# Performance work log

Hardware: AMD Instinct MI355X
Metric: run time of the kernel (lower is better)

The kernel has to match this reference:

```python
import jax, jax.numpy as jnp
import numpy as np

N, E, G = 40000, 400000, 64
IN, ED, HID, HEADS, OUT = 2, 18, 64, 4, 3

def _glorot(key, shape):
    fan_in = shape[0]
    return jax.random.normal(key, shape, dtype=jnp.float32) / np.float32(np.sqrt(fan_in))

def setup_inputs():
    key = jax.random.key(0)
    ks = jax.random.split(key, 32)
    d1 = HEADS * HID  # 256
    return {
        "x": jax.random.normal(ks[0], (N, IN), jnp.float32),
        "edge_index": jax.random.randint(ks[1], (2, E), 0, N),
        "edge_attr": jax.random.normal(ks[2], (E, ED), jnp.float32),
        "batch": jnp.sort(jax.random.randint(ks[3], (N,), 0, G)),
        # conv1: TransformerConv(2 -> 64, heads=4, concat=True, beta=True, edge_dim=18)
        "Wq1": _glorot(ks[4], (IN, d1)), "bq1": jnp.zeros((d1,), jnp.float32),
        "Wk1": _glorot(ks[5], (IN, d1)), "bk1": jnp.zeros((d1,), jnp.float32),
        "Wv1": _glorot(ks[6], (IN, d1)), "bv1": jnp.zeros((d1,), jnp.float32),
        "We1": _glorot(ks[7], (ED, d1)),
        "Wskip1": _glorot(ks[8], (IN, d1)), "bskip1": jnp.zeros((d1,), jnp.float32),
        "Wbeta1": _glorot(ks[9], (3 * d1, 1)),
        # conv2: TransformerConv(256 -> 64, heads=1, concat=False, beta=True, edge_dim=18)
        "Wq2": _glorot(ks[10], (d1, HID)), "bq2": jnp.zeros((HID,), jnp.float32),
        "Wk2": _glorot(ks[11], (d1, HID)), "bk2": jnp.zeros((HID,), jnp.float32),
        "Wv2": _glorot(ks[12], (d1, HID)), "bv2": jnp.zeros((HID,), jnp.float32),
        "We2": _glorot(ks[13], (ED, HID)),
        "Wskip2": _glorot(ks[14], (d1, HID)), "bskip2": jnp.zeros((HID,), jnp.float32),
        "Wbeta2": _glorot(ks[15], (3 * HID, 1)),
        "Wlin": _glorot(ks[16], (HID, OUT)), "blin": jnp.zeros((OUT,), jnp.float32),
    }

def _tconv(x, src, dst, edge_attr, Wq, bq, Wk, bk, Wv, bv, We, Wskip, bskip, Wbeta, H, C, concat):
    # PyG TransformerConv with edge_dim, beta=True, root_weight=True (eval: dropout off)
    n = x.shape[0]
    q = (x @ Wq + bq).reshape(n, H, C)
    k = (x @ Wk + bk).reshape(n, H, C)
    v = (x @ Wv + bv).reshape(n, H, C)
    e = (edge_attr @ We).reshape(-1, H, C)              # [E,H,C]
    kj = k[src] + e                                      # key_j + edge
    alpha = jnp.einsum('ehc,ehc->eh', q[dst], kj) * (1.0 / (C ** 0.5))  # [E,H]
    # segment softmax over destination nodes
    amax = jax.ops.segment_max(alpha, dst, num_segments=n)
    ex = jnp.exp(alpha - amax[dst])
    den = jax.ops.segment_sum(ex, dst, num_segments=n)
    w = ex / (den[dst] + 1e-16)
    msg = (v[src] + e) * w[:, :, None]                   # [E,H,C]
    out = jax.ops.segment_sum(msg, dst, num_segments=n)  # [N,H,C]
    out = out.reshape(n, H * C) if concat else out.mean(axis=1)
    # beta-gated skip connection
    xr = x @ Wskip + bskip
    beta = jax.nn.sigmoid(jnp.concatenate([out, xr, out - xr], axis=-1) @ Wbeta)
    return beta * xr + (1.0 - beta) * out

def reference(x, edge_index, edge_attr, batch, Wq1, bq1, Wk1, bk1, Wv1, bv1, We1, Wskip1, bskip1, Wbeta1, Wq2, bq2, Wk2, bk2, Wv2, bv2, We2, Wskip2, bskip2, Wbeta2, Wlin, blin):
    src, dst = edge_index[0], edge_index[1]
    h = jax.nn.relu(_tconv(x, src, dst, edge_attr, Wq1, bq1, Wk1, bk1, Wv1, bv1, We1, Wskip1, bskip1, Wbeta1, HEADS, HID, True))
    h = jax.nn.relu(_tconv(h, src, dst, edge_attr, Wq2, bq2, Wk2, bk2, Wv2, bv2, We2, Wskip2, bskip2, Wbeta2, 1, HID, False))
    # global mean pool per graph
    s = jax.ops.segment_sum(h, batch, num_segments=G)
    cnt = jax.ops.segment_sum(jnp.ones((h.shape[0], 1), h.dtype), batch, num_segments=G)
    pooled = s / jnp.maximum(cnt, 1.0)
    return pooled @ Wlin + blin
```

## Files before the change

### kernel.cpp

```cpp
#include <hip/hip_runtime.h>
#include <hip/hip_fp16.h>

#define N_NODES 40000
#define N_EDGES 400000
#define N_GRAPHS 64
#define D1 256
#define HIDC 64
#define NHEADS 4
#define EDIM 18
#define EPAD 20
#define OUTF 3
#define APAD 264

typedef _Float16 f16x8 __attribute__((ext_vector_type(8)));
typedef float f32x4 __attribute__((ext_vector_type(4)));

__global__ void prep_w(const float* __restrict__ Wq, const float* __restrict__ bq,
                       const float* __restrict__ Wk, const float* __restrict__ bk,
                       const float* __restrict__ Wv, const float* __restrict__ bv,
                       const float* __restrict__ Ws, const float* __restrict__ bs,
                       const float* __restrict__ We2,
                       const float* __restrict__ Wq1, const float* __restrict__ bq1,
                       const float* __restrict__ Wk1, const float* __restrict__ bk1,
                       const float* __restrict__ We1,
                       __half* __restrict__ Bt, float* __restrict__ bias,
                       float* __restrict__ cbuf) {
    int c = blockIdx.x, k = threadIdx.x;
    if (c < 256) {
        int m = c >> 6, d = c & 63;
        const float* W = (m == 0) ? Wq : (m == 1) ? Wk : (m == 2) ? Wv : Ws;
        Bt[c * 256 + k] = __float2half(W[k * 64 + d]);
        if (k == 0) {
            const float* b = (m == 0) ? bq : (m == 1) ? bk : (m == 2) ? bv : bs;
            bias[c] = b[d];
        }
    } else if (c < 288) {
        int j = c - 256;
        float s = 0.f;
        if (j < EDIM)
            for (int cc = 0; cc < 64; ++cc) s += Wq[k * 64 + cc] * We2[j * 64 + cc];
        Bt[c * 256 + k] = __float2half(s);
        if (k == 0) {
            float b = 0.f;
            if (j < EDIM)
                for (int cc = 0; cc < 64; ++cc) b += bq[cc] * We2[j * 64 + cc];
            bias[c] = b;
        }
    } else {
        int t = k;
        if (t < 36) {
            int h = t / 9, r = t % 9, a = r / 3, b = r % 3;
            const float* A = (a == 0) ? Wq1 : (a == 1) ? Wq1 + D1 : bq1;
            const float* B = (b == 0) ? Wk1 : (b == 1) ? Wk1 + D1 : bk1;
            float s = 0.f;
            for (int cc = 0; cc < 64; ++cc) s += A[h * 64 + cc] * B[h * 64 + cc];
            cbuf[h * 63 + a * 3 + b] = s;
        } else if (t < 252) {
            int i = t - 36;
            int h = i / 54, rr = (i % 54) / 18, j = i % 18;
            const float* A = (rr == 0) ? Wq1 : (rr == 1) ? Wq1 + D1 : bq1;
            float s = 0.f;
            for (int cc = 0; cc < 64; ++cc) s += A[h * 64 + cc] * We1[j * D1 + h * 64 + cc];
            cbuf[h * 63 + 9 + rr * 18 + j] = s;
        }
    }
}

__global__ void initA(const float* __restrict__ x, const float* __restrict__ cbuf,
                      float* __restrict__ coef, float* __restrict__ acc1,
                      float* __restrict__ acc2, float* __restrict__ out2,
                      int* __restrict__ deg, float* __restrict__ pooled,
                      int* __restrict__ gs, int* __restrict__ ge) {
    int t = blockIdx.x * 256 + threadIdx.x;
    acc1[t] = 0.f;
    {
        int n = t / 84, r = t % 84, h = r / 21, c = r % 21;
        const float* cb = cbuf + h * 63;
        float x0 = x[2 * n], x1 = x[2 * n + 1], o;
        if (c < 3) o = x0 * cb[c] + x1 * cb[3 + c] + cb[6 + c];
        else { int j = c - 3; o = x0 * cb[9 + j] + x1 * cb[27 + j] + cb[45 + j]; }
        coef[t] = o;
    }
    if (t < N_NODES * 64) out2[t] = 0.f;
    if (t < N_NODES * 20) acc2[t] = 0.f;
    if (t < N_NODES) deg[t] = 0;
    if (t < N_GRAPHS * HIDC) pooled[t] = 0.f;
    if (t < N_GRAPHS) { gs[t] = 0; ge[t] = 0; }
}

__global__ void hist_kernel(const int* __restrict__ ei, int* __restrict__ deg,
                            const int* __restrict__ batch, int* __restrict__ gs,
                            int* __restrict__ ge) {
    int e = blockIdx.x * 256 + threadIdx.x;
    if (e < N_EDGES) atomicAdd(&deg[ei[N_EDGES + e]], 1);
    int n = e;
    if (n < N_NODES) {
        int b = batch[n];
        if (n == 0) gs[b] = 0;
        else { int pb = batch[n - 1]; if (pb != b) { ge[pb] = n; gs[b] = n; } }
        if (n == N_NODES - 1) ge[b] = N_NODES;
    }
}

__global__ void scanA(const int* __restrict__ deg, int* __restrict__ bsum) {
    __shared__ int s[256];
    int b = blockIdx.x, t = threadIdx.x;
    s[t] = (t < 160) ? deg[b * 160 + t] : 0;
    __syncthreads();
    for (int off = 128; off; off >>= 1) {
        if (t < off) s[t] += s[t + off];
        __syncthreads();
    }
    if (t == 0) bsum[b] = s[0];
}

__global__ void scanB(const int* __restrict__ bsum, int* __restrict__ boff) {
    __shared__ int s[256];
    int t = threadIdx.x;
    int v = (t < 250) ? bsum[t] : 0;
    s[t] = v;
    __syncthreads();
    for (int off = 1; off < 256; off <<= 1) {
        int add = (t >= off) ? s[t - off] : 0;
        __syncthreads();
        s[t] += add;
        __syncthreads();
    }
    if (t < 250) boff[t] = s[t] - v;
}

__global__ void scanC(const int* __restrict__ deg, const int* __restrict__ boff,
                      int* __restrict__ cursor) {
    __shared__ int s[256];
    int b = blockIdx.x, t = threadIdx.x;
    int v = (t < 160) ? deg[b * 160 + t] : 0;
    s[t] = v;
    __syncthreads();
    for (int off = 1; off < 256; off <<= 1) {
        int add = (t >= off) ? s[t - off] : 0;
        __syncthreads();
        s[t] += add;
        __syncthreads();
    }
    if (t < 160) cursor[b * 160 + t] = boff[b] + s[t] - v;
}

__global__ void scatterE(const int* __restrict__ ei, const float* __restrict__ ea,
                         const float* __restrict__ x, int* __restrict__ cursor,
                         int* __restrict__ src_s, int* __restrict__ dst_s,
                         float* __restrict__ ea_s) {
    int e = blockIdx.x * 256 + threadIdx.x;
    if (e >= N_EDGES) return;
    int src = ei[e], dst = ei[N_EDGES + e];
    const float2* sr = (const float2*)(ea + (size_t)e * EDIM);
    float2 s0 = sr[0], s1 = sr[1], s2 = sr[2], s3 = sr[3], s4 = sr[4],
           s5 = sr[5], s6 = sr[6], s7 = sr[7], s8 = sr[8];
    float2 xv = *(const float2*)(x + (size_t)src * 2);
    int p = atomicAdd(&cursor[dst], 1);
    src_s[p] = src;
    dst_s[p] = dst;
    float4* drow = (float4*)(ea_s + (size_t)p * EPAD);
    drow[0] = make_float4(s0.x, s0.y, s1.x, s1.y);
    drow[1] = make_float4(s2.x, s2.y, s3.x, s3.y);
    drow[2] = make_float4(s4.x, s4.y, s5.x, s5.y);
    drow[3] = make_float4(s6.x, s6.y, s7.x, s7.y);
    drow[4] = make_float4(s8.x, s8.y, xv.x, xv.y);
}

__global__ void strip1f(const int* __restrict__ dst_s, const float* __restrict__ ea_s,
                        const float* __restrict__ coef, float* __restrict__ acc1) {
    int t = threadIdx.x;
    int strip = blockIdx.x * 2 + (t >> 7);
    int l = t & 127;
    int h = l >> 5, comp = l & 31;
    bool active = comp < 21;
    int voff = (comp == 0) ? 18 : (comp == 1) ? 19 : (comp >= 3 ? comp - 3 : 0);
    bool isone = (comp == 2);
    int cidx = h * 21 + comp;
    int p0 = strip * 16;
    int dsts[16]; float v[16];
    #pragma unroll
    for (int j = 0; j < 16; ++j) dsts[j] = dst_s[p0 + j];
    #pragma unroll
    for (int j = 0; j < 16; ++j)
        v[j] = active ? (isone ? 1.f : ea_s[(size_t)(p0 + j) * EPAD + voff]) : 0.f;
    int prev = dsts[0];
    float c = active ? coef[(size_t)prev * 84 + cidx] : 0.f;
    float acc = 0.f;
    #pragma unroll
    for (int j = 0; j < 16; ++j) {
        if (dsts[j] != prev) {
            if (active) atomicAdd(&acc1[(size_t)prev * 84 + cidx], acc);
            acc = 0.f; prev = dsts[j];
            c = active ? coef[(size_t)prev * 84 + cidx] : 0.f;
        }
        float prod = c * v[j];
        #pragma unroll
        for (int off = 16; off; off >>= 1) prod += __shfl_xor(prod, off);
        float w = __expf(prod * 0.125f);
        acc += w * v[j];
    }
    if (active) atomicAdd(&acc1[(size_t)prev * 84 + cidx], acc);
}

__global__ void finalize1x(const float* __restrict__ x, const float* __restrict__ acc1,
                           const float* __restrict__ Wv, const float* __restrict__ bv,
                           const float* __restrict__ We, const float* __restrict__ Wskip,
                           const float* __restrict__ bskip, const float* __restrict__ Wbeta,
                           __half* __restrict__ h1f) {
    __shared__ float red[4][4];
    int nb = blockIdx.x * 4;
    int t = threadIdx.x;
    int h = t >> 6;
    float wv0 = Wv[t], wv1 = Wv[D1 + t], bvv = bv[t];
    float we[EDIM];
    #pragma unroll
    for (int j = 0; j < EDIM; ++j) we[j] = We[j * D1 + t];
    float ws0 = Wskip[t], ws1 = Wskip[D1 + t], bsv = bskip[t];
    float wb0 = Wbeta[t], wb1 = Wbeta[D1 + t], wb2 = Wbeta[2 * D1 + t];
    float o[4], xr[4], part[4];
    #pragma unroll
    for (int i = 0; i < 4; ++i) {
        int node = nb + i;
        const float* a = acc1 + (size_t)node * 84 + h * 21;
        float l = a[2];
        float oo = a[0] * wv0 + a[1] * wv1 + l * bvv;
        #pragma unroll
        for (int j = 0; j < EDIM; ++j) oo += a[3 + j] * we[j];
        oo /= (l + 1e-16f);
        float x0 = x[node * 2], x1 = x[node * 2 + 1];
        xr[i] = x0 * ws0 + x1 * ws1 + bsv;
        o[i] = oo;
        part[i] = oo * wb0 + xr[i] * wb1 + (oo - xr[i]) * wb2;
    }
    #pragma unroll
    for (int off = 32; off; off >>= 1) {
        #pragma unroll
        for (int i = 0; i < 4; ++i) part[i] += __shfl_xor(part[i], off);
    }
    if ((t & 63) == 0) {
        #pragma unroll
        for (int i = 0; i < 4; ++i) red[h][i] = part[i];
    }
    __syncthreads();
    #pragma unroll
    for (int i = 0; i < 4; ++i) {
        float tot = red[0][i] + red[1][i] + red[2][i] + red[3][i];
        float beta = 1.f / (1.f + __expf(-tot));
        h1f[(size_t)(nb + i) * D1 + t] =
            __float2half(fmaxf(beta * xr[i] + (1.f - beta) * o[i], 0.f));
    }
}

__device__ __forceinline__ void nl2_store(int c, int gr, float v,
        float* __restrict__ q2, float* __restrict__ k2, __half* __restrict__ v2h,
        float* __restrict__ xr2, float* __restrict__ qe) {
    if (c < 256) {
        int m = c >> 6, d = c & 63;
        if (m == 0)      q2[(size_t)gr * 64 + d] = v;
        else if (m == 1) k2[(size_t)gr * 64 + d] = v;
        else if (m == 2) v2h[(size_t)gr * 64 + d] = __float2half(v);
        else             xr2[(size_t)gr * 64 + d] = v;
    } else {
        qe[(size_t)gr * 32 + (c - 256)] = v;
    }
}

__global__ __launch_bounds__(256) void nl2_mfma(
        const __half* __restrict__ h1f, const __half* __restrict__ Bt,
        const float* __restrict__ bias,
        float* __restrict__ q2, float* __restrict__ k2,
        __half* __restrict__ v2h, float* __restrict__ xr2,
        float* __restrict__ qe) {
    __shared__ _Float16 As[64 * APAD];
    int t = threadIdx.x;
    int row0 = blockIdx.x * 64;
    const float4* gsrc = (const float4*)(h1f + (size_t)row0 * 256);
    #pragma unroll
    for (int i = 0; i < 8; ++i) {
        int li = i * 256 + t;
        int r = li >> 5, c8 = li & 31;
        *(float4*)(As + r * APAD + c8 * 8) = gsrc[li];
    }
    __syncthreads();
    int wave = t >> 6, lane = t & 63, quad = lane >> 4, mm = lane & 15;
    const _Float16* Bp = (const _Float16*)Bt;
    for (int ct = wave; ct < 18; ct += 4) {
        int c0 = ct * 16 + mm;
        const _Float16* b0 = Bp + (size_t)c0 * 256 + quad * 8;
        f16x8 b[8];
        #pragma unroll
        for (int s = 0; s < 8; ++s) b[s] = *(const f16x8*)(b0 + s * 32);
        float bz = bias[c0];
        #pragma unroll
        for (int rt = 0; rt < 4; ++rt) {
            const _Float16* arow = As + (rt * 16 + mm) * APAD + quad * 8;
            f16x8 a[8];
            #pragma unroll
            for (int s = 0; s < 8; ++s) a[s] = *(const f16x8*)(arow + s * 32);
            f32x4 accA = {bz, bz, bz, bz};
            f32x4 accB = {0.f, 0.f, 0.f, 0.f};
            #pragma unroll
            for (int s = 0; s < 4; ++s) {
                accA = __builtin_amdgcn_mfma_f32_16x16x32_f16(a[s],     b[s],     accA, 0, 0, 0);
                accB = __builtin_amdgcn_mfma_f32_16x16x32_f16(a[s + 4], b[s + 4], accB, 0, 0, 0);
            }
            #pragma unroll
            for (int r = 0; r < 4; ++r) {
                int gr = row0 + rt * 16 + quad * 4 + r;
                nl2_store(c0, gr, accA[r] + accB[r], q2, k2, v2h, xr2, qe);
            }
        }
    }
}

#define LG2_BLOCKS 2048
#define LG2_WAVES (LG2_BLOCKS * 4)
__global__ void logits2(const int* __restrict__ src_s, const int* __restrict__ dst_s,
                        const float* __restrict__ ea_s, const float* __restrict__ q2,
                        const float* __restrict__ k2, const float* __restrict__ qe,
                        float* __restrict__ alpha2) {
    int t = threadIdx.x, wid = t >> 6, lane = t & 63;
    int w = blockIdx.x * 4 + wid;
    for (int base = w; base < N_EDGES; base += 2 * LG2_WAVES) {
        int p1 = base, p2 = base + LG2_WAVES;
        bool has2 = p2 < N_EDGES;
        int p2c = has2 ? p2 : p1;
        int s1 = src_s[p1], d1 = dst_s[p1];
        int s2 = src_s[p2c], d2 = dst_s[p2c];
        float dd1 = q2[(size_t)d1 * 64 + lane] * k2[(size_t)s1 * 64 + lane];
        float dd2 = q2[(size_t)d2 * 64 + lane] * k2[(size_t)s2 * 64 + lane];
        if (lane < 20) {
            dd1 += qe[(size_t)d1 * 32 + lane] * ea_s[(size_t)p1 * EPAD + lane];
            dd2 += qe[(size_t)d2 * 32 + lane] * ea_s[(size_t)p2c * EPAD + lane];
        }
        #pragma unroll
        for (int off = 32; off; off >>= 1) {
            dd1 += __shfl_xor(dd1, off);
            dd2 += __shfl_xor(dd2, off);
        }
        if (lane == 0) {
            alpha2[p1] = __expf(dd1 * 0.125f);
            if (has2) alpha2[p2] = __expf(dd2 * 0.125f);
        }
    }
}

__global__ void spmm2s(const int* __restrict__ dst_s, const int* __restrict__ src_s,
                       const float* __restrict__ alpha2, const __half* __restrict__ v2h,
                       const float* __restrict__ ea_s,
                       float* __restrict__ out2, float* __restrict__ acc2) {
    int t = threadIdx.x;
    int strip = blockIdx.x * 4 + (t >> 6);
    int lane = t & 63;
    int p0 = strip * 16;
    int dsts[16]; int srcs[16]; float w[16];
    #pragma unroll
    for (int j = 0; j < 16; ++j) dsts[j] = dst_s[p0 + j];
    #pragma unroll
    for (int j = 0; j < 16; ++j) srcs[j] = src_s[p0 + j];
    #pragma unroll
    for (int j = 0; j < 16; ++j) w[j] = alpha2[p0 + j];
    float vv[16]; float ev[16];
    #pragma unroll
    for (int j = 0; j < 16; ++j) vv[j] = __half2float(v2h[(size_t)srcs[j] * 64 + lane]);
    #pragma unroll
    for (int j = 0; j < 16; ++j)
        ev[j] = (lane < EDIM) ? ea_s[(size_t)(p0 + j) * EPAD + lane] : 1.f;
    float acc = 0.f, accS = 0.f;
    int prev = dsts[0];
    #pragma unroll
    for (int j = 0; j < 16; ++j) {
        if (dsts[j] != prev) {
            atomicAdd(&out2[(size_t)prev * 64 + lane], acc);
            if (lane < 19) atomicAdd(&acc2[(size_t)prev * 20 + lane], accS);
            acc = 0.f; accS = 0.f; prev = dsts[j];
        }
        acc += w[j] * vv[j];
        accS += w[j] * ev[j];
    }
    atomicAdd(&out2[(size_t)prev * 64 + lane], acc);
    if (lane < 19) atomicAdd(&acc2[(size_t)prev * 20 + lane], accS);
}

__global__ void finalize2x(const float* __restrict__ out2, const float* __restrict__ acc2,
                           const float* __restrict__ xr2, const float* __restrict__ We2,
                           const float* __restrict__ Wb2, float* __restrict__ h2) {
    __shared__ float w2s[EDIM * 64];
    int t = threadIdx.x;
    for (int i = t; i < EDIM * 64; i += 256) w2s[i] = We2[i];
    __syncthreads();
    int node = blockIdx.x * 4 + (t >> 6);
    int lane = t & 63;
    const float* a2 = acc2 + (size_t)node * 20;
    float num = out2[(size_t)node * 64 + lane];
    #pragma unroll
    for (int j = 0; j < EDIM; ++j) num += a2[j] * w2s[j * 64 + lane];
    float o = num / (a2[18] + 1e-16f);
    float xr = xr2[(size_t)node * 64 + lane];
    float part = o * Wb2[lane] + xr * Wb2[64 + lane] + (o - xr) * Wb2[128 + lane];
    #pragma unroll
    for (int off = 32; off; off >>= 1) part += __shfl_xor(part, off);
    float beta = 1.f / (1.f + __expf(-part));
    h2[(size_t)node * 64 + lane] = fmaxf(beta * xr + (1.f - beta) * o, 0.f);
}

__global__ void pool_kernel(const float* __restrict__ h2, const int* __restrict__ gs,
                            const int* __restrict__ ge, float* __restrict__ pooled) {
    __shared__ float red[4][64];
    int g = blockIdx.x >> 2, q = blockIdx.x & 3;
    int t = threadIdx.x, wv = t >> 6, lane = t & 63;
    int s = gs[g], e = ge[g];
    float sum = 0.f;
    for (int n = s + q * 4 + wv; n < e; n += 16) sum += h2[(size_t)n * 64 + lane];
    red[wv][lane] = sum;
    __syncthreads();
    if (wv == 0) {
        float v = red[0][lane] + red[1][lane] + red[2][lane] + red[3][lane];
        atomicAdd(&pooled[g * 64 + lane], v);
    }
}

__global__ void final_lin(const float* __restrict__ pooled, const int* __restrict__ gs,
                          const int* __restrict__ ge,
                          const float* __restrict__ Wlin, const float* __restrict__ blin,
                          float* __restrict__ out) {
    int t = threadIdx.x;
    if (t >= N_GRAPHS * OUTF) return;
    int g = t / OUTF, o = t % OUTF;
    int c = ge[g] - gs[g];
    float inv = 1.f / fmaxf((float)c, 1.f);
    float acc = 0.f;
    for (int kk = 0; kk < HIDC; ++kk) acc += pooled[g * 64 + kk] * Wlin[kk * OUTF + o];
    out[t] = acc * inv + blin[o];
}

extern "C" void kernel_launch(void* const* d_in, const int* in_sizes, int n_in,
                              void* d_out, int out_size, void* d_ws, size_t ws_size,
                              hipStream_t stream) {
    const float* x      = (const float*)d_in[0];
    const int*   ei     = (const int*)d_in[1];
    const float* ea     = (const float*)d_in[2];
    const int*   batch  = (const int*)d_in[3];
    const float* Wq1    = (const float*)d_in[4];  const float* bq1    = (const float*)d_in[5];
    const float* Wk1    = (const float*)d_in[6];  const float* bk1    = (const float*)d_in[7];
    const float* Wv1    = (const float*)d_in[8];  const float* bv1    = (const float*)d_in[9];
    const float* We1    = (const float*)d_in[10];
    const float* Wskip1 = (const float*)d_in[11]; const float* bskip1 = (const float*)d_in[12];
    const float* Wbeta1 = (const float*)d_in[13];
    const float* Wq2    = (const float*)d_in[14]; const float* bq2    = (const float*)d_in[15];
    const float* Wk2    = (const float*)d_in[16]; const float* bk2    = (const float*)d_in[17];
    const float* Wv2    = (const float*)d_in[18]; const float* bv2    = (const float*)d_in[19];
    const float* We2    = (const float*)d_in[20];
    const float* Wskip2 = (const float*)d_in[21]; const float* bskip2 = (const float*)d_in[22];
    const float* Wbeta2 = (const float*)d_in[23];
    const float* Wlin   = (const float*)d_in[24]; const float* blin   = (const float*)d_in[25];

    float* ptr = (float*)d_ws;
    float* q2     = ptr; ptr += (size_t)N_NODES * 64;
    float* k2     = ptr; ptr += (size_t)N_NODES * 64;
    float* xr2    = ptr; ptr += (size_t)N_NODES * 64;
    float* qe     = ptr; ptr += (size_t)N_NODES * 32;
    __half* v2h   = (__half*)ptr; ptr += (size_t)N_NODES * 32;
    float* ea_s   = ptr; ptr += (size_t)N_EDGES * EPAD;
    float* alpha2 = ptr; ptr += N_EDGES;
    float* acc2   = ptr; ptr += (size_t)N_NODES * 20;
    float* out2   = ptr; ptr += (size_t)N_NODES * 64;
    float* pooled = ptr; ptr += N_GRAPHS * HIDC;
    int*   gs     = (int*)ptr; ptr += N_GRAPHS;
    int*   ge     = (int*)ptr; ptr += N_GRAPHS;
    float* cbuf   = ptr; ptr += 256;
    float* bias   = ptr; ptr += 320;
    __half* Bt    = (__half*)ptr; ptr += (288 * 256) / 2;
    int*   src_s  = (int*)ptr; ptr += N_EDGES;
    int*   dst_s  = (int*)ptr; ptr += N_EDGES;
    int*   deg    = (int*)ptr; ptr += N_NODES;
    int*   cursor = (int*)ptr; ptr += N_NODES;
    int*   bsum   = (int*)ptr; ptr += 256;
    int*   boff   = (int*)ptr; ptr += 256;
    float* coef   = ptr; ptr += (size_t)N_NODES * 84;
    float* h2     = coef;
    float* acc1   = ptr; ptr += (size_t)N_NODES * 84;
    __half* h1f   = (__half*)ptr; ptr += (size_t)N_NODES * 128;

    const int EB = (N_EDGES + 255) / 256;

    prep_w<<<289, 256, 0, stream>>>(Wq2, bq2, Wk2, bk2, Wv2, bv2, Wskip2, bskip2, We2,
                                    Wq1, bq1, Wk1, bk1, We1, Bt, bias, cbuf);
    initA<<<(N_NODES * 84) / 256, 256, 0, stream>>>(x, cbuf, coef, acc1, acc2, out2,
                                                    deg, pooled, gs, ge);
    hist_kernel<<<EB, 256, 0, stream>>>(ei, deg, batch, gs, ge);
    scanA<<<250, 256, 0, stream>>>(deg, bsum);
    scanB<<<1, 256, 0, stream>>>(bsum, boff);
    scanC<<<250, 256, 0, stream>>>(deg, boff, cursor);
    scatterE<<<EB, 256, 0, stream>>>(ei, ea, x, cursor, src_s, dst_s, ea_s);

    strip1f<<<(N_EDGES / 16) / 2, 256, 0, stream>>>(dst_s, ea_s, coef, acc1);
    finalize1x<<<N_NODES / 4, 256, 0, stream>>>(x, acc1, Wv1, bv1, We1, Wskip1, bskip1,
                                                Wbeta1, h1f);

    nl2_mfma<<<N_NODES / 64, 256, 0, stream>>>(h1f, Bt, bias, q2, k2, v2h, xr2, qe);
    logits2<<<LG2_BLOCKS, 256, 0, stream>>>(src_s, dst_s, ea_s, q2, k2, qe, alpha2);
    spmm2s<<<(N_EDGES / 16) / 4, 256, 0, stream>>>(dst_s, src_s, alpha2, v2h, ea_s,
                                                   out2, acc2);
    finalize2x<<<N_NODES / 4, 256, 0, stream>>>(out2, acc2, xr2, We2, Wbeta2, h2);

    pool_kernel<<<N_GRAPHS * 4, 256, 0, stream>>>(h2, gs, ge, pooled);
    final_lin<<<1, 256, 0, stream>>>(pooled, gs, ge, Wlin, blin, (float*)d_out);
}
```

Measured before the change: 425.5 us.

## Compute layer-1 attention weights per edge in scatter and store them in edge rows

Moves the layer-1 per-head attention logit and exp computation from strip1f into scatterE. Each edge computes its own weights from the precomputed coefficient buffer and the src/dst features, and writes four weights into the sorted edge row, which is widened from 20 to 32 floats. This removes the per-node coef array, its fill in initA, and the shuffle reductions in strip1f. In exchange, every layer-2 kernel that reads ea_s now reads wider rows, and scatterE does more arithmetic per edge, with each thread handling two edges.

```diff
diff --git a/kernel.cpp b/kernel.cpp
--- a/kernel.cpp
+++ b/kernel.cpp
@@ -8,7 +8,7 @@
 #define HIDC 64
 #define NHEADS 4
 #define EDIM 18
-#define EPAD 20
+#define EPAD 32
 #define OUTF 3
 #define APAD 264
 
@@ -66,21 +66,12 @@
     }
 }
 
-__global__ void initA(const float* __restrict__ x, const float* __restrict__ cbuf,
-                      float* __restrict__ coef, float* __restrict__ acc1,
-                      float* __restrict__ acc2, float* __restrict__ out2,
-                      int* __restrict__ deg, float* __restrict__ pooled,
+__global__ void initA(float* __restrict__ acc1, float* __restrict__ acc2,
+                      float* __restrict__ out2, int* __restrict__ deg,
+                      float* __restrict__ pooled,
                       int* __restrict__ gs, int* __restrict__ ge) {
     int t = blockIdx.x * 256 + threadIdx.x;
     acc1[t] = 0.f;
-    {
-        int n = t / 84, r = t % 84, h = r / 21, c = r % 21;
-        const float* cb = cbuf + h * 63;
-        float x0 = x[2 * n], x1 = x[2 * n + 1], o;
-        if (c < 3) o = x0 * cb[c] + x1 * cb[3 + c] + cb[6 + c];
-        else { int j = c - 3; o = x0 * cb[9 + j] + x1 * cb[27 + j] + cb[45 + j]; }
-        coef[t] = o;
-    }
     if (t < N_NODES * 64) out2[t] = 0.f;
     if (t < N_NODES * 20) acc2[t] = 0.f;
     if (t < N_NODES) deg[t] = 0;
@@ -146,29 +137,69 @@
 }
 
 __global__ void scatterE(const int* __restrict__ ei, const float* __restrict__ ea,
-                         const float* __restrict__ x, int* __restrict__ cursor,
+                         const float* __restrict__ x, const float* __restrict__ cbuf,
+                         int* __restrict__ cursor,
                          int* __restrict__ src_s, int* __restrict__ dst_s,
                          float* __restrict__ ea_s) {
-    int e = blockIdx.x * 256 + threadIdx.x;
-    if (e >= N_EDGES) return;
-    int src = ei[e], dst = ei[N_EDGES + e];
-    const float2* sr = (const float2*)(ea + (size_t)e * EDIM);
-    float2 s0 = sr[0], s1 = sr[1], s2 = sr[2], s3 = sr[3], s4 = sr[4],
-           s5 = sr[5], s6 = sr[6], s7 = sr[7], s8 = sr[8];
-    float2 xv = *(const float2*)(x + (size_t)src * 2);
-    int p = atomicAdd(&cursor[dst], 1);
-    src_s[p] = src;
-    dst_s[p] = dst;
-    float4* drow = (float4*)(ea_s + (size_t)p * EPAD);
-    drow[0] = make_float4(s0.x, s0.y, s1.x, s1.y);
-    drow[1] = make_float4(s2.x, s2.y, s3.x, s3.y);
-    drow[2] = make_float4(s4.x, s4.y, s5.x, s5.y);
-    drow[3] = make_float4(s6.x, s6.y, s7.x, s7.y);
-    drow[4] = make_float4(s8.x, s8.y, xv.x, xv.y);
+    __shared__ float cb[252];
+    int t = threadIdx.x;
+    if (t < 252) cb[t] = cbuf[t];
+    __syncthreads();
+    const int HALF = N_EDGES / 2;
+    int e0 = blockIdx.x * 256 + t;
+    if (e0 >= HALF) return;
+    int eA = e0, eB = e0 + HALF;
+    int srcA = ei[eA], dstA = ei[N_EDGES + eA];
+    int srcB = ei[eB], dstB = ei[N_EDGES + eB];
+    int pA = atomicAdd(&cursor[dstA], 1);
+    int pB = atomicAdd(&cursor[dstB], 1);
+    #pragma unroll
+    for (int half = 0; half < 2; ++half) {
+        int e   = half ? eB : eA;
+        int src = half ? srcB : srcA;
+        int dst = half ? dstB : dstA;
+        int p   = half ? pB : pA;
+        const float2* sr = (const float2*)(ea + (size_t)e * EDIM);
+        float s[EDIM];
+        #pragma unroll
+        for (int j = 0; j < 9; ++j) {
+            float2 v2 = sr[j];
+            s[2 * j] = v2.x; s[2 * j + 1] = v2.y;
+        }
+        float2 xs = *(const float2*)(x + (size_t)src * 2);
+        float2 xd = *(const float2*)(x + (size_t)dst * 2);
+        float w[NHEADS];
+        #pragma unroll
+        for (int h = 0; h < NHEADS; ++h) {
+            const float* c = cb + h * 63;
+            float ta[3];
+            #pragma unroll
+            for (int a = 0; a < 3; ++a) {
+                float tv = c[a * 3] * xs.x + c[a * 3 + 1] * xs.y + c[a * 3 + 2];
+                const float* cc = c + 9 + a * 18;
+                #pragma unroll
+                for (int j = 0; j < EDIM; ++j) tv += cc[j] * s[j];
+                ta[a] = tv;
+            }
+            float alpha = xd.x * ta[0] + xd.y * ta[1] + ta[2];
+            w[h] = __expf(alpha * 0.125f);
+        }
+        src_s[p] = src;
+        dst_s[p] = dst;
+        float4* drow = (float4*)(ea_s + (size_t)p * EPAD);
+        drow[0] = make_float4(s[0],  s[1],  s[2],  s[3]);
+        drow[1] = make_float4(s[4],  s[5],  s[6],  s[7]);
+        drow[2] = make_float4(s[8],  s[9],  s[10], s[11]);
+        drow[3] = make_float4(s[12], s[13], s[14], s[15]);
+        drow[4] = make_float4(s[16], s[17], xs.x, xs.y);
+        drow[5] = make_float4(w[0], w[1], w[2], w[3]);
+        drow[6] = make_float4(0.f, 0.f, 0.f, 0.f);
+        drow[7] = make_float4(0.f, 0.f, 0.f, 0.f);
+    }
 }
 
 __global__ void strip1f(const int* __restrict__ dst_s, const float* __restrict__ ea_s,
-                        const float* __restrict__ coef, float* __restrict__ acc1) {
+                        float* __restrict__ acc1) {
     int t = threadIdx.x;
     int strip = blockIdx.x * 2 + (t >> 7);
     int l = t & 127;
@@ -178,27 +209,23 @@
     bool isone = (comp == 2);
     int cidx = h * 21 + comp;
     int p0 = strip * 16;
-    int dsts[16]; float v[16];
+    int dsts[16]; float v[16]; float w[16];
     #pragma unroll
     for (int j = 0; j < 16; ++j) dsts[j] = dst_s[p0 + j];
+    #pragma unroll
+    for (int j = 0; j < 16; ++j) w[j] = ea_s[(size_t)(p0 + j) * EPAD + 20 + h];
     #pragma unroll
     for (int j = 0; j < 16; ++j)
         v[j] = active ? (isone ? 1.f : ea_s[(size_t)(p0 + j) * EPAD + voff]) : 0.f;
+    float acc = 0.f;
     int prev = dsts[0];
-    float c = active ? coef[(size_t)prev * 84 + cidx] : 0.f;
-    float acc = 0.f;
     #pragma unroll
     for (int j = 0; j < 16; ++j) {
         if (dsts[j] != prev) {
             if (active) atomicAdd(&acc1[(size_t)prev * 84 + cidx], acc);
             acc = 0.f; prev = dsts[j];
-            c = active ? coef[(size_t)prev * 84 + cidx] : 0.f;
-        }
-        float prod = c * v[j];
-        #pragma unroll
-        for (int off = 16; off; off >>= 1) prod += __shfl_xor(prod, off);
-        float w = __expf(prod * 0.125f);
-        acc += w * v[j];
+        }
+        acc += w[j] * v[j];
     }
     if (active) atomicAdd(&acc1[(size_t)prev * 84 + cidx], acc);
 }
@@ -478,8 +505,7 @@
     int*   cursor = (int*)ptr; ptr += N_NODES;
     int*   bsum   = (int*)ptr; ptr += 256;
     int*   boff   = (int*)ptr; ptr += 256;
-    float* coef   = ptr; ptr += (size_t)N_NODES * 84;
-    float* h2     = coef;
+    float* h2     = ptr; ptr += (size_t)N_NODES * 84;
     float* acc1   = ptr; ptr += (size_t)N_NODES * 84;
     __half* h1f   = (__half*)ptr; ptr += (size_t)N_NODES * 128;
 
@@ -487,15 +513,15 @@
 
     prep_w<<<289, 256, 0, stream>>>(Wq2, bq2, Wk2, bk2, Wv2, bv2, Wskip2, bskip2, We2,
                                     Wq1, bq1, Wk1, bk1, We1, Bt, bias, cbuf);
-    initA<<<(N_NODES * 84) / 256, 256, 0, stream>>>(x, cbuf, coef, acc1, acc2, out2,
-                                                    deg, pooled, gs, ge);
+    initA<<<(N_NODES * 84) / 256, 256, 0, stream>>>(acc1, acc2, out2, deg, pooled, gs, ge);
     hist_kernel<<<EB, 256, 0, stream>>>(ei, deg, batch, gs, ge);
     scanA<<<250, 256, 0, stream>>>(deg, bsum);
     scanB<<<1, 256, 0, stream>>>(bsum, boff);
     scanC<<<250, 256, 0, stream>>>(deg, boff, cursor);
-    scatterE<<<EB, 256, 0, stream>>>(ei, ea, x, cursor, src_s, dst_s, ea_s);
-
-    strip1f<<<(N_EDGES / 16) / 2, 256, 0, stream>>>(dst_s, ea_s, coef, acc1);
+    scatterE<<<(N_EDGES / 2 + 255) / 256, 256, 0, stream>>>(ei, ea, x, cbuf, cursor,
+                                                            src_s, dst_s, ea_s);
+
+    strip1f<<<(N_EDGES / 16) / 2, 256, 0, stream>>>(dst_s, ea_s, acc1);
     finalize1x<<<N_NODES / 4, 256, 0, stream>>>(x, acc1, Wv1, bv1, We1, Wskip1, bskip1,
                                                 Wbeta1, h1f);
 
```

Result: slower. 659.3 us (+54.9%).

## Compute layer-1 attention weights per edge in a dedicated kernel before aggregation

Applied to the files above, without the earlier changes.

Layer-1 attention exponentials are no longer built from a per-node coefficient table and a wavefront shuffle reduction inside the strip aggregation kernel. A new per-edge kernel computes all four head weights from the folded query/key/edge constants in shared memory and writes them to a buffer. The strip kernel then only does weighted accumulation. This removes the shuffle reductions and redundant exp work at the cost of an extra launch and a 6.4 MB write and read of per-edge weights.

```diff
diff --git a/kernel.cpp b/kernel.cpp
--- a/kernel.cpp
+++ b/kernel.cpp
@@ -66,21 +66,12 @@
     }
 }
 
-__global__ void initA(const float* __restrict__ x, const float* __restrict__ cbuf,
-                      float* __restrict__ coef, float* __restrict__ acc1,
-                      float* __restrict__ acc2, float* __restrict__ out2,
-                      int* __restrict__ deg, float* __restrict__ pooled,
+__global__ void initA(float* __restrict__ acc1, float* __restrict__ acc2,
+                      float* __restrict__ out2, int* __restrict__ deg,
+                      float* __restrict__ pooled,
                       int* __restrict__ gs, int* __restrict__ ge) {
     int t = blockIdx.x * 256 + threadIdx.x;
     acc1[t] = 0.f;
-    {
-        int n = t / 84, r = t % 84, h = r / 21, c = r % 21;
-        const float* cb = cbuf + h * 63;
-        float x0 = x[2 * n], x1 = x[2 * n + 1], o;
-        if (c < 3) o = x0 * cb[c] + x1 * cb[3 + c] + cb[6 + c];
-        else { int j = c - 3; o = x0 * cb[9 + j] + x1 * cb[27 + j] + cb[45 + j]; }
-        coef[t] = o;
-    }
     if (t < N_NODES * 64) out2[t] = 0.f;
     if (t < N_NODES * 20) acc2[t] = 0.f;
     if (t < N_NODES) deg[t] = 0;
@@ -167,8 +158,46 @@
     drow[4] = make_float4(s8.x, s8.y, xv.x, xv.y);
 }
 
+__global__ void logits1(const int* __restrict__ dst_s, const float* __restrict__ ea_s,
+                        const float* __restrict__ x, const float* __restrict__ cbuf,
+                        float* __restrict__ w1) {
+    __shared__ float cb[252];
+    int t = threadIdx.x;
+    if (t < 252) cb[t] = cbuf[t];
+    __syncthreads();
+    int p = blockIdx.x * 256 + t;
+    if (p >= N_EDGES) return;
+    const float4* row = (const float4*)(ea_s + (size_t)p * EPAD);
+    float4 r0 = row[0], r1 = row[1], r2 = row[2], r3 = row[3], r4 = row[4];
+    float s[EDIM];
+    s[0]=r0.x; s[1]=r0.y; s[2]=r0.z; s[3]=r0.w;
+    s[4]=r1.x; s[5]=r1.y; s[6]=r1.z; s[7]=r1.w;
+    s[8]=r2.x; s[9]=r2.y; s[10]=r2.z; s[11]=r2.w;
+    s[12]=r3.x; s[13]=r3.y; s[14]=r3.z; s[15]=r3.w;
+    s[16]=r4.x; s[17]=r4.y;
+    float xs0 = r4.z, xs1 = r4.w;
+    int dst = dst_s[p];
+    float2 xd = *(const float2*)(x + (size_t)dst * 2);
+    float w[NHEADS];
+    #pragma unroll
+    for (int h = 0; h < NHEADS; ++h) {
+        const float* c = cb + h * 63;
+        float alpha = 0.f;
+        #pragma unroll
+        for (int a = 0; a < 3; ++a) {
+            float tv = c[a * 3] * xs0 + c[a * 3 + 1] * xs1 + c[a * 3 + 2];
+            const float* cc = c + 9 + a * 18;
+            #pragma unroll
+            for (int j = 0; j < EDIM; ++j) tv += cc[j] * s[j];
+            alpha += tv * ((a == 0) ? xd.x : (a == 1) ? xd.y : 1.f);
+        }
+        w[h] = __expf(alpha * 0.125f);
+    }
+    *(float4*)(w1 + (size_t)p * 4) = make_float4(w[0], w[1], w[2], w[3]);
+}
+
 __global__ void strip1f(const int* __restrict__ dst_s, const float* __restrict__ ea_s,
-                        const float* __restrict__ coef, float* __restrict__ acc1) {
+                        const float* __restrict__ w1, float* __restrict__ acc1) {
     int t = threadIdx.x;
     int strip = blockIdx.x * 2 + (t >> 7);
     int l = t & 127;
@@ -178,27 +207,23 @@
     bool isone = (comp == 2);
     int cidx = h * 21 + comp;
     int p0 = strip * 16;
-    int dsts[16]; float v[16];
+    int dsts[16]; float v[16]; float w[16];
     #pragma unroll
     for (int j = 0; j < 16; ++j) dsts[j] = dst_s[p0 + j];
+    #pragma unroll
+    for (int j = 0; j < 16; ++j) w[j] = w1[(size_t)(p0 + j) * 4 + h];
     #pragma unroll
     for (int j = 0; j < 16; ++j)
         v[j] = active ? (isone ? 1.f : ea_s[(size_t)(p0 + j) * EPAD + voff]) : 0.f;
+    float acc = 0.f;
     int prev = dsts[0];
-    float c = active ? coef[(size_t)prev * 84 + cidx] : 0.f;
-    float acc = 0.f;
     #pragma unroll
     for (int j = 0; j < 16; ++j) {
         if (dsts[j] != prev) {
             if (active) atomicAdd(&acc1[(size_t)prev * 84 + cidx], acc);
             acc = 0.f; prev = dsts[j];
-            c = active ? coef[(size_t)prev * 84 + cidx] : 0.f;
-        }
-        float prod = c * v[j];
-        #pragma unroll
-        for (int off = 16; off; off >>= 1) prod += __shfl_xor(prod, off);
-        float w = __expf(prod * 0.125f);
-        acc += w * v[j];
+        }
+        acc += w[j] * v[j];
     }
     if (active) atomicAdd(&acc1[(size_t)prev * 84 + cidx], acc);
 }
@@ -478,8 +503,8 @@
     int*   cursor = (int*)ptr; ptr += N_NODES;
     int*   bsum   = (int*)ptr; ptr += 256;
     int*   boff   = (int*)ptr; ptr += 256;
-    float* coef   = ptr; ptr += (size_t)N_NODES * 84;
-    float* h2     = coef;
+    float* w1     = ptr; ptr += (size_t)N_EDGES * 4;
+    float* h2     = ptr; ptr += (size_t)N_NODES * 84;
     float* acc1   = ptr; ptr += (size_t)N_NODES * 84;
     __half* h1f   = (__half*)ptr; ptr += (size_t)N_NODES * 128;
 
@@ -487,15 +512,15 @@
 
     prep_w<<<289, 256, 0, stream>>>(Wq2, bq2, Wk2, bk2, Wv2, bv2, Wskip2, bskip2, We2,
                                     Wq1, bq1, Wk1, bk1, We1, Bt, bias, cbuf);
-    initA<<<(N_NODES * 84) / 256, 256, 0, stream>>>(x, cbuf, coef, acc1, acc2, out2,
-                                                    deg, pooled, gs, ge);
+    initA<<<(N_NODES * 84) / 256, 256, 0, stream>>>(acc1, acc2, out2, deg, pooled, gs, ge);
     hist_kernel<<<EB, 256, 0, stream>>>(ei, deg, batch, gs, ge);
     scanA<<<250, 256, 0, stream>>>(deg, bsum);
     scanB<<<1, 256, 0, stream>>>(bsum, boff);
     scanC<<<250, 256, 0, stream>>>(deg, boff, cursor);
     scatterE<<<EB, 256, 0, stream>>>(ei, ea, x, cursor, src_s, dst_s, ea_s);
 
-    strip1f<<<(N_EDGES / 16) / 2, 256, 0, stream>>>(dst_s, ea_s, coef, acc1);
+    logits1<<<EB, 256, 0, stream>>>(dst_s, ea_s, x, cbuf, w1);
+    strip1f<<<(N_EDGES / 16) / 2, 256, 0, stream>>>(dst_s, ea_s, w1, acc1);
     finalize1x<<<N_NODES / 4, 256, 0, stream>>>(x, acc1, Wv1, bv1, We1, Wskip1, bskip1,
                                                 Wbeta1, h1f);
 
```

Result: faster. 416.0 us (-2.2%).
